# Performance work log

Hardware: AMD Instinct MI355X
Metric: run time of the kernel (lower is better)

## Reference

```python
import jax, jax.numpy as jnp
import numpy as np

D_MODEL, D_HID, N_EXPERTS, TOP_K = 1024, 4096, 8, 2

def setup_inputs() -> dict:
    key = jax.random.key(0)
    ks = jax.random.split(key, 6)
    B, T = 2, 2048
    x = jax.random.normal(ks[0], (B, T, D_MODEL), dtype=jnp.float32)
    gate_w = jax.random.normal(ks[1], (N_EXPERTS, D_MODEL), dtype=jnp.float32) * (1.0 / np.sqrt(D_MODEL))
    # kaiming_uniform-ish init for expert weights
    lim1 = np.sqrt(6.0 / D_MODEL)
    lim2 = np.sqrt(6.0 / D_HID)
    w1 = jax.random.uniform(ks[2], (N_EXPERTS, D_MODEL, D_HID), dtype=jnp.float32, minval=-lim1, maxval=lim1)
    w2 = jax.random.uniform(ks[3], (N_EXPERTS, D_HID, D_MODEL), dtype=jnp.float32, minval=-lim2, maxval=lim2)
    b1 = jnp.zeros((N_EXPERTS, 1, D_HID), dtype=jnp.float32)
    b2 = jnp.zeros((N_EXPERTS, 1, D_MODEL), dtype=jnp.float32)
    return {"x": x, "gate_w": gate_w, "w1": w1, "b1": b1, "w2": w2, "b2": b2}

def reference(x, gate_w, w1, b1, w2, b2):
    B, T, D = x.shape
    E = gate_w.shape[0]
    xf = x.reshape(-1, D)                              # [N, D]
    N = xf.shape[0]
    # Router: logits -> softmax -> top-k -> renormalize
    logits = jnp.einsum('nd,ed->ne', xf, gate_w)       # [N, E]
    scores = jax.nn.softmax(logits, axis=-1)
    top_w, top_i = jax.lax.top_k(scores, TOP_K)        # [N, K]
    top_w = top_w / jnp.sum(top_w, axis=-1, keepdims=True)
    # Dense combine weights (zero for unselected experts) — same math as
    # the padded-bmm dispatch/combine: padded slots have weight 0.
    gates = jnp.zeros((N, E), xf.dtype).at[jnp.arange(N)[:, None], top_i].add(top_w)  # [N, E]
    # Grouped expert MLP (computed densely; weighted combine zeroes unrouted experts)
    h = jax.nn.gelu(jnp.einsum('nd,edh->enh', xf, w1) + b1, approximate=False)  # [E, N, H]
    expert_out = jnp.einsum('enh,ehd->end', h, w2) + b2                          # [E, N, D]
    out = jnp.einsum('end,ne->nd', expert_out, gates)                            # [N, D]
    return out.reshape(B, T, D)
```

## Files before the change

kernel.cpp:

```cpp
#include <hip/hip_runtime.h>
#include <math.h>

#define NTOK 4096
#define DM   1024
#define DH   4096
#define NE   8
#define NSLOT (NTOK*2)
#define TMAX 72

typedef unsigned short u16;
typedef __attribute__((ext_vector_type(8))) short shortx8;
typedef __attribute__((ext_vector_type(4))) float floatx4;
typedef __attribute__((ext_vector_type(4))) int   intx4;

__device__ __forceinline__ u16 f2bf(float f) {
  union { float f; unsigned u; } c; c.f = f;
  unsigned r = c.u + 0x7fffu + ((c.u >> 16) & 1u);
  return (u16)(r >> 16);
}

__device__ __forceinline__ void async_cp16(const u16* g, u16* l) {
  __builtin_amdgcn_global_load_lds(
      (const __attribute__((address_space(1))) void*)g,
      (__attribute__((address_space(3))) void*)l, 16, 0, 0);
}

__global__ void cvt_x_kernel(const float* __restrict__ x, u16* __restrict__ xb) {
  int i = (blockIdx.x * 256 + threadIdx.x) * 8;
  float4 v0 = *(const float4*)(x + i);
  float4 v1 = *(const float4*)(x + i + 4);
  u16 tmp[8] = {f2bf(v0.x), f2bf(v0.y), f2bf(v0.z), f2bf(v0.w),
                f2bf(v1.x), f2bf(v1.y), f2bf(v1.z), f2bf(v1.w)};
  *(intx4*)(xb + i) = *(intx4*)tmp;
}

template<int K, int NW>
__global__ __launch_bounds__(256) void transpose_kernel(const float* __restrict__ W,
                                                        u16* __restrict__ Wt) {
  __shared__ u16 tile[64][66];
  int e = blockIdx.z;
  int n0 = blockIdx.x * 64, k0 = blockIdx.y * 64;
  int tt = threadIdx.x;
  const float* src = W + (size_t)e * K * NW + (size_t)(k0 + (tt >> 2)) * NW + n0 + (tt & 3) * 16;
  int r = tt >> 2, c4 = (tt & 3) * 16;
  float4 v[4];
#pragma unroll
  for (int i = 0; i < 4; i++) v[i] = *(const float4*)(src + i * 4);
#pragma unroll
  for (int i = 0; i < 4; i++) {
    tile[r][c4 + 4 * i + 0] = f2bf(v[i].x);
    tile[r][c4 + 4 * i + 1] = f2bf(v[i].y);
    tile[r][c4 + 4 * i + 2] = f2bf(v[i].z);
    tile[r][c4 + 4 * i + 3] = f2bf(v[i].w);
  }
  __syncthreads();
  u16* dst = Wt + (size_t)e * NW * K + (size_t)n0 * K + k0;
#pragma unroll
  for (int p = 0; p < 2; p++) {
    int n = (tt >> 3) + p * 32;
    int kc = (tt & 7) * 8;
    u16 o[8];
#pragma unroll
    for (int i = 0; i < 8; i++) o[i] = tile[kc + i][n];
    *(intx4*)(dst + (size_t)n * K + kc) = *(intx4*)o;
  }
}

__global__ __launch_bounds__(256) void router_kernel(const float* __restrict__ x,
                                                     const float* __restrict__ gw,
                                                     int* __restrict__ eos,
                                                     float* __restrict__ wos) {
  int wave = threadIdx.x >> 6, lane = threadIdx.x & 63;
  int n = blockIdx.x * 4 + wave;
  const float* xr = x + (size_t)n * DM;
  float acc[NE];
#pragma unroll
  for (int e = 0; e < NE; e++) acc[e] = 0.f;
  for (int d = lane; d < DM; d += 64) {
    float xv = xr[d];
#pragma unroll
    for (int e = 0; e < NE; e++) acc[e] += xv * gw[e * DM + d];
  }
#pragma unroll
  for (int e = 0; e < NE; e++) {
    float v = acc[e];
#pragma unroll
    for (int off = 32; off > 0; off >>= 1) v += __shfl_xor(v, off, 64);
    acc[e] = v;
  }
  if (lane == 0) {
    int i0 = 0;
    for (int e = 1; e < NE; e++) if (acc[e] > acc[i0]) i0 = e;
    int i1 = (i0 == 0) ? 1 : 0;
    for (int e = 0; e < NE; e++) { if (e == i0) continue; if (acc[e] > acc[i1]) i1 = e; }
    float e1 = expf(acc[i1] - acc[i0]);
    float w0 = 1.f / (1.f + e1);
    eos[2 * n] = i0;  eos[2 * n + 1] = i1;
    wos[2 * n] = w0;  wos[2 * n + 1] = 1.f - w0;
  }
}

__global__ __launch_bounds__(256) void build_groups_kernel(
    const int* __restrict__ eos, const float* __restrict__ wos,
    int* __restrict__ goff, int* __restrict__ tok_of_g, float* __restrict__ w_of_g,
    int* __restrict__ tiles, int* __restrict__ ntiles) {
  __shared__ int pref[256][NE];
  __shared__ int tot[NE];
  __shared__ int ebase[NE + 1];
  int t = threadIdx.x;
  int c[NE];
#pragma unroll
  for (int e = 0; e < NE; e++) c[e] = 0;
  for (int i = 0; i < NSLOT / 256; i++) {
    int e = eos[t * (NSLOT / 256) + i];
#pragma unroll
    for (int q = 0; q < NE; q++) if (e == q) c[q]++;
  }
#pragma unroll
  for (int e = 0; e < NE; e++) pref[t][e] = c[e];
  __syncthreads();
  if (t < NE) {
    int run = 0;
    for (int i = 0; i < 256; i++) { int v = pref[i][t]; pref[i][t] = run; run += v; }
    tot[t] = run;
  }
  __syncthreads();
  if (t == 0) {
    int o = 0;
    for (int e = 0; e < NE; e++) { ebase[e] = o; o += tot[e]; }
    ebase[NE] = o;
    int nt = 0;
    for (int e = 0; e < NE; e++)
      for (int mb = 0; mb * 128 < tot[e]; mb++) tiles[nt++] = (e << 16) | mb;
    ntiles[0] = nt;
  }
  __syncthreads();
  int off[NE];
#pragma unroll
  for (int e = 0; e < NE; e++) off[e] = ebase[e] + pref[t][e];
  for (int i = 0; i < NSLOT / 256; i++) {
    int s = t * (NSLOT / 256) + i;
    int e = eos[s];
    int g = 0;
#pragma unroll
    for (int q = 0; q < NE; q++) if (e == q) { g = off[q]; off[q] = g + 1; }
    tok_of_g[g] = s >> 1;
    w_of_g[g] = wos[s];
  }
  if (t <= NE) goff[t] = ebase[t];
}

template<int K, int NOUT, int MODE, int KSPLIT>
__global__ __launch_bounds__(256) void moe_gemm(
    const u16* __restrict__ A, const u16* __restrict__ Wt, const float* __restrict__ bias,
    const int* __restrict__ goff, const int* __restrict__ tok_of_g,
    const float* __restrict__ w_of_g, const int* __restrict__ tiles,
    const int* __restrict__ ntiles,
    u16* __restrict__ Hout, float* __restrict__ Out) {
  const int KLEN = K / KSPLIT;
  const int NB = NOUT / 128;
  const int NWG = TMAX * NB * KSPLIT;
  int flat = blockIdx.x;
  int wgid = (flat & 7) * (NWG >> 3) + (flat >> 3);
  int nb   = wgid % NB;
  int rest = wgid / NB;
  int tl   = rest % TMAX;
  int kseg = rest / TMAX;
  if (tl >= ntiles[0]) return;
  int packed = tiles[tl];
  int e = packed >> 16;
  int mb = packed & 0xffff;
  int gb = goff[e];
  int cntE = goff[e + 1] - gb;
  int m0 = mb * 128;
  int mvalid = cntE - m0; if (mvalid > 128) mvalid = 128;
  int gbase = gb + m0;
  int n0 = nb * 128;
  int kbeg = kseg * KLEN;
  int tid = threadIdx.x;
  int lane = tid & 63, wave = tid >> 6;

  __shared__ __align__(16) u16 As[2][128 * 64];
  __shared__ __align__(16) u16 Bs[2][128 * 64];

  int gcol = (((lane & 7) ^ (lane >> 3)) * 8);
  const u16 *pA[4], *pB[4];
  const u16* wte = Wt + (size_t)e * NOUT * K;
#pragma unroll
  for (int i = 0; i < 4; i++) {
    int rw = wave * 32 + i * 8 + (lane >> 3);
    int cw = (rw < mvalid) ? rw : (mvalid - 1);
    if (MODE == 0) pA[i] = A + (size_t)tok_of_g[gbase + cw] * K + gcol;
    else           pA[i] = A + (size_t)(gbase + cw) * K + gcol;
    pB[i] = wte + (size_t)(n0 + rw) * K + gcol;
  }

  int wm = wave >> 1, wn = wave & 1;
  int lr = lane & 15;
  int c0 = (((lane >> 4)) ^ (lr & 7)) * 8;
  int c1 = ((4 + (lane >> 4)) ^ (lr & 7)) * 8;

  floatx4 acc[4][4];
#pragma unroll
  for (int i = 0; i < 4; i++)
#pragma unroll
    for (int j = 0; j < 4; j++) acc[i][j] = (floatx4){0.f, 0.f, 0.f, 0.f};

  auto stage = [&](int b, int k0) {
#pragma unroll
    for (int i = 0; i < 4; i++)
      async_cp16(pA[i] + k0, &As[b][(wave * 32 + i * 8) * 64]);
#pragma unroll
    for (int i = 0; i < 4; i++)
      async_cp16(pB[i] + k0, &Bs[b][(wave * 32 + i * 8) * 64]);
  };

  const int NT = KLEN / 64;
  stage(0, kbeg);
  stage(1, kbeg + 64);

  shortx8 af[8], bfr[8];
  auto ldfrag_half = [&](int b, int h) {
    int cc = h ? c1 : c0;
#pragma unroll
    for (int i = 0; i < 4; i++) {
      af[h * 4 + i]  = *(const shortx8*)&As[b][(wm * 64 + i * 16 + lr) * 64 + cc];
      bfr[h * 4 + i] = *(const shortx8*)&Bs[b][(wn * 64 + i * 16 + lr) * 64 + cc];
    }
  };
  auto mfma_half = [&](int h) {
#pragma unroll
    for (int i = 0; i < 4; i++)
#pragma unroll
      for (int j = 0; j < 4; j++)
        acc[i][j] = __builtin_amdgcn_mfma_f32_16x16x32_bf16(af[h * 4 + i], bfr[h * 4 + j],
                                                            acc[i][j], 0, 0, 0);
  };

  for (int t = 0; t < NT - 2; ++t) {
    int cur = t & 1;
    asm volatile("s_waitcnt vmcnt(8)" ::: "memory");
    __builtin_amdgcn_s_barrier();
    asm volatile("" ::: "memory");
    ldfrag_half(cur, 0);
    asm volatile("" ::: "memory");
    ldfrag_half(cur, 1);
    asm volatile("s_waitcnt lgkmcnt(8)" ::: "memory");
    __builtin_amdgcn_sched_barrier(0);
    __builtin_amdgcn_s_setprio(1);
    mfma_half(0);
    __builtin_amdgcn_s_setprio(0);
    asm volatile("s_waitcnt lgkmcnt(0)" ::: "memory");
    __builtin_amdgcn_sched_barrier(0);
    __builtin_amdgcn_s_barrier();
    __builtin_amdgcn_sched_barrier(0);
    stage(cur, kbeg + (t + 2) * 64);
    __builtin_amdgcn_sched_barrier(0);
    __builtin_amdgcn_s_setprio(1);
    mfma_half(1);
    __builtin_amdgcn_s_setprio(0);
  }
#pragma unroll
  for (int tt2 = 0; tt2 < 2; ++tt2) {
    int cur = (NT + tt2) & 1;
    if (tt2 == 0) asm volatile("s_waitcnt vmcnt(8)" ::: "memory");
    else          asm volatile("s_waitcnt vmcnt(0)" ::: "memory");
    __builtin_amdgcn_s_barrier();
    asm volatile("" ::: "memory");
    ldfrag_half(cur, 0);
    asm volatile("" ::: "memory");
    ldfrag_half(cur, 1);
    asm volatile("s_waitcnt lgkmcnt(8)" ::: "memory");
    __builtin_amdgcn_sched_barrier(0);
    mfma_half(0);
    asm volatile("s_waitcnt lgkmcnt(0)" ::: "memory");
    __builtin_amdgcn_sched_barrier(0);
    mfma_half(1);
  }

  const float* bp = bias + (size_t)e * NOUT + n0;
  if (MODE == 0) {
#pragma unroll
    for (int i = 0; i < 4; i++) {
      int rowb = wm * 64 + i * 16 + (lane >> 4) * 4;
#pragma unroll
      for (int r = 0; r < 4; r++) {
        int grow = rowb + r;
        if (grow < mvalid) {
          size_t base = (size_t)(gbase + grow) * NOUT + n0;
#pragma unroll
          for (int j = 0; j < 4; j++) {
            int col = wn * 64 + j * 16 + lr;
            float v = acc[i][j][r] + bp[col];
            v = 0.5f * v * (1.f + erff(v * 0.70710678118654752f));
            Hout[base + col] = f2bf(v);
          }
        }
      }
    }
  } else {
#pragma unroll
    for (int i = 0; i < 4; i++) {
      int rowb = wm * 64 + i * 16 + (lane >> 4) * 4;
#pragma unroll
      for (int r = 0; r < 4; r++) {
        int grow = rowb + r;
        if (grow < mvalid) {
          int gi = gbase + grow;
          int t = tok_of_g[gi];
          float wg = w_of_g[gi];
          float* orow = Out + (size_t)t * DM + n0;
#pragma unroll
          for (int j = 0; j < 4; j++) {
            int col = wn * 64 + j * 16 + lr;
            float bb = (kseg == 0) ? bp[col] : 0.f;
            atomicAdd(&orow[col], wg * (acc[i][j][r] + bb));
          }
        }
      }
    }
  }
}

extern "C" void kernel_launch(void* const* d_in, const int* in_sizes, int n_in,
                              void* d_out, int out_size, void* d_ws, size_t ws_size,
                              hipStream_t stream) {
  const float* x  = (const float*)d_in[0];
  const float* gw = (const float*)d_in[1];
  const float* w1 = (const float*)d_in[2];
  const float* b1 = (const float*)d_in[3];
  const float* w2 = (const float*)d_in[4];
  const float* b2 = (const float*)d_in[5];
  float* out = (float*)d_out;
  char* ws = (char*)d_ws;

  u16* xb = (u16*)(ws + 0);
  u16* wt = (u16*)(ws + 8388608);
  u16* h  = (u16*)(ws + 75497472);
  char* meta = ws + 142606336;
  int*   eos      = (int*)(meta);
  int*   tok_of_g = (int*)(meta + 32768);
  float* wos      = (float*)(meta + 65536);
  float* w_of_g   = (float*)(meta + 98304);
  int*   goff     = (int*)(meta + 131072);
  int*   tiles    = (int*)(meta + 131200);
  int*   ntiles   = (int*)(meta + 131584);

  hipMemsetAsync(out, 0, (size_t)NTOK * DM * 4, stream);

  cvt_x_kernel<<<NTOK * DM / 8 / 256, 256, 0, stream>>>(x, xb);
  transpose_kernel<DM, DH><<<dim3(DH / 64, DM / 64, NE), 256, 0, stream>>>(w1, wt);
  router_kernel<<<NTOK / 4, 256, 0, stream>>>(x, gw, eos, wos);
  build_groups_kernel<<<1, 256, 0, stream>>>(eos, wos, goff, tok_of_g, w_of_g, tiles, ntiles);
  moe_gemm<DM, DH, 0, 1><<<TMAX * (DH / 128), 256, 0, stream>>>(
      xb, wt, b1, goff, tok_of_g, w_of_g, tiles, ntiles, h, nullptr);
  transpose_kernel<DH, DM><<<dim3(DM / 64, DH / 64, NE), 256, 0, stream>>>(w2, wt);
  moe_gemm<DH, DM, 1, 2><<<TMAX * (DM / 128) * 2, 256, 0, stream>>>(
      h, wt, b2, goff, tok_of_g, w_of_g, tiles, ntiles, nullptr, out);
}
```

Baseline: 714.7 us.

## Enlarge MoE GEMM tiles to 256x256 with 512-thread workgroups

```diff
diff --git a/kernel.cpp b/kernel.cpp
--- a/kernel.cpp
+++ b/kernel.cpp
@@ -6,7 +6,7 @@
 #define DH   4096
 #define NE   8
 #define NSLOT (NTOK*2)
-#define TMAX 72
+#define TM   40
 
 typedef unsigned short u16;
 typedef __attribute__((ext_vector_type(8))) short shortx8;
@@ -131,7 +131,7 @@
     ebase[NE] = o;
     int nt = 0;
     for (int e = 0; e < NE; e++)
-      for (int mb = 0; mb * 128 < tot[e]; mb++) tiles[nt++] = (e << 16) | mb;
+      for (int mb = 0; mb * 256 < tot[e]; mb++) tiles[nt++] = (e << 16) | mb;
     ntiles[0] = nt;
   }
   __syncthreads();
@@ -151,37 +151,37 @@
 }
 
 template<int K, int NOUT, int MODE, int KSPLIT>
-__global__ __launch_bounds__(256) void moe_gemm(
+__global__ __launch_bounds__(512, 2) void moe_gemm(
     const u16* __restrict__ A, const u16* __restrict__ Wt, const float* __restrict__ bias,
     const int* __restrict__ goff, const int* __restrict__ tok_of_g,
     const float* __restrict__ w_of_g, const int* __restrict__ tiles,
     const int* __restrict__ ntiles,
     u16* __restrict__ Hout, float* __restrict__ Out) {
   const int KLEN = K / KSPLIT;
-  const int NB = NOUT / 128;
-  const int NWG = TMAX * NB * KSPLIT;
+  const int NB = NOUT / 256;
+  const int NWG = TM * NB * KSPLIT;
   int flat = blockIdx.x;
   int wgid = (flat & 7) * (NWG >> 3) + (flat >> 3);
   int nb   = wgid % NB;
   int rest = wgid / NB;
-  int tl   = rest % TMAX;
-  int kseg = rest / TMAX;
+  int tl   = rest % TM;
+  int kseg = rest / TM;
   if (tl >= ntiles[0]) return;
   int packed = tiles[tl];
   int e = packed >> 16;
   int mb = packed & 0xffff;
   int gb = goff[e];
   int cntE = goff[e + 1] - gb;
-  int m0 = mb * 128;
-  int mvalid = cntE - m0; if (mvalid > 128) mvalid = 128;
+  int m0 = mb * 256;
+  int mvalid = cntE - m0; if (mvalid > 256) mvalid = 256;
   int gbase = gb + m0;
-  int n0 = nb * 128;
+  int n0 = nb * 256;
   int kbeg = kseg * KLEN;
   int tid = threadIdx.x;
   int lane = tid & 63, wave = tid >> 6;
 
-  __shared__ __align__(16) u16 As[2][128 * 64];
-  __shared__ __align__(16) u16 Bs[2][128 * 64];
+  __shared__ __align__(16) u16 As[2][256 * 64];
+  __shared__ __align__(16) u16 Bs[2][256 * 64];
 
   int gcol = (((lane & 7) ^ (lane >> 3)) * 8);
   const u16 *pA[4], *pB[4];
@@ -195,14 +195,14 @@
     pB[i] = wte + (size_t)(n0 + rw) * K + gcol;
   }
 
-  int wm = wave >> 1, wn = wave & 1;
+  int wm = wave >> 2, wn = wave & 3;
   int lr = lane & 15;
   int c0 = (((lane >> 4)) ^ (lr & 7)) * 8;
   int c1 = ((4 + (lane >> 4)) ^ (lr & 7)) * 8;
 
-  floatx4 acc[4][4];
-#pragma unroll
-  for (int i = 0; i < 4; i++)
+  floatx4 acc[8][4];
+#pragma unroll
+  for (int i = 0; i < 8; i++)
 #pragma unroll
     for (int j = 0; j < 4; j++) acc[i][j] = (floatx4){0.f, 0.f, 0.f, 0.f};
 
@@ -219,22 +219,22 @@
   stage(0, kbeg);
   stage(1, kbeg + 64);
 
-  shortx8 af[8], bfr[8];
+  shortx8 af[8], bfr[4];
   auto ldfrag_half = [&](int b, int h) {
     int cc = h ? c1 : c0;
 #pragma unroll
-    for (int i = 0; i < 4; i++) {
-      af[h * 4 + i]  = *(const shortx8*)&As[b][(wm * 64 + i * 16 + lr) * 64 + cc];
-      bfr[h * 4 + i] = *(const shortx8*)&Bs[b][(wn * 64 + i * 16 + lr) * 64 + cc];
-    }
+    for (int i = 0; i < 8; i++)
+      af[i]  = *(const shortx8*)&As[b][(wm * 128 + i * 16 + lr) * 64 + cc];
+#pragma unroll
+    for (int j = 0; j < 4; j++)
+      bfr[j] = *(const shortx8*)&Bs[b][(wn * 64 + j * 16 + lr) * 64 + cc];
   };
-  auto mfma_half = [&](int h) {
-#pragma unroll
-    for (int i = 0; i < 4; i++)
+  auto mfma_half = [&]() {
+#pragma unroll
+    for (int i = 0; i < 8; i++)
 #pragma unroll
       for (int j = 0; j < 4; j++)
-        acc[i][j] = __builtin_amdgcn_mfma_f32_16x16x32_bf16(af[h * 4 + i], bfr[h * 4 + j],
-                                                            acc[i][j], 0, 0, 0);
+        acc[i][j] = __builtin_amdgcn_mfma_f32_16x16x32_bf16(af[i], bfr[j], acc[i][j], 0, 0, 0);
   };
 
   for (int t = 0; t < NT - 2; ++t) {
@@ -243,21 +243,20 @@
     __builtin_amdgcn_s_barrier();
     asm volatile("" ::: "memory");
     ldfrag_half(cur, 0);
-    asm volatile("" ::: "memory");
+    asm volatile("s_waitcnt lgkmcnt(0)" ::: "memory");
+    __builtin_amdgcn_sched_barrier(0);
+    __builtin_amdgcn_s_setprio(1);
+    mfma_half();
+    __builtin_amdgcn_s_setprio(0);
     ldfrag_half(cur, 1);
-    asm volatile("s_waitcnt lgkmcnt(8)" ::: "memory");
+    asm volatile("s_waitcnt lgkmcnt(0)" ::: "memory");
+    __builtin_amdgcn_sched_barrier(0);
+    __builtin_amdgcn_s_barrier();
+    __builtin_amdgcn_sched_barrier(0);
+    stage(cur, kbeg + (t + 2) * 64);
     __builtin_amdgcn_sched_barrier(0);
     __builtin_amdgcn_s_setprio(1);
-    mfma_half(0);
-    __builtin_amdgcn_s_setprio(0);
-    asm volatile("s_waitcnt lgkmcnt(0)" ::: "memory");
-    __builtin_amdgcn_sched_barrier(0);
-    __builtin_amdgcn_s_barrier();
-    __builtin_amdgcn_sched_barrier(0);
-    stage(cur, kbeg + (t + 2) * 64);
-    __builtin_amdgcn_sched_barrier(0);
-    __builtin_amdgcn_s_setprio(1);
-    mfma_half(1);
+    mfma_half();
     __builtin_amdgcn_s_setprio(0);
   }
 #pragma unroll
@@ -268,21 +267,20 @@
     __builtin_amdgcn_s_barrier();
     asm volatile("" ::: "memory");
     ldfrag_half(cur, 0);
-    asm volatile("" ::: "memory");
+    asm volatile("s_waitcnt lgkmcnt(0)" ::: "memory");
+    __builtin_amdgcn_sched_barrier(0);
+    mfma_half();
     ldfrag_half(cur, 1);
-    asm volatile("s_waitcnt lgkmcnt(8)" ::: "memory");
-    __builtin_amdgcn_sched_barrier(0);
-    mfma_half(0);
     asm volatile("s_waitcnt lgkmcnt(0)" ::: "memory");
     __builtin_amdgcn_sched_barrier(0);
-    mfma_half(1);
+    mfma_half();
   }
 
   const float* bp = bias + (size_t)e * NOUT + n0;
   if (MODE == 0) {
 #pragma unroll
-    for (int i = 0; i < 4; i++) {
-      int rowb = wm * 64 + i * 16 + (lane >> 4) * 4;
+    for (int i = 0; i < 8; i++) {
+      int rowb = wm * 128 + i * 16 + (lane >> 4) * 4;
 #pragma unroll
       for (int r = 0; r < 4; r++) {
         int grow = rowb + r;
@@ -300,8 +298,8 @@
     }
   } else {
 #pragma unroll
-    for (int i = 0; i < 4; i++) {
-      int rowb = wm * 64 + i * 16 + (lane >> 4) * 4;
+    for (int i = 0; i < 8; i++) {
+      int rowb = wm * 128 + i * 16 + (lane >> 4) * 4;
 #pragma unroll
       for (int r = 0; r < 4; r++) {
         int grow = rowb + r;
@@ -352,9 +350,9 @@
   transpose_kernel<DM, DH><<<dim3(DH / 64, DM / 64, NE), 256, 0, stream>>>(w1, wt);
   router_kernel<<<NTOK / 4, 256, 0, stream>>>(x, gw, eos, wos);
   build_groups_kernel<<<1, 256, 0, stream>>>(eos, wos, goff, tok_of_g, w_of_g, tiles, ntiles);
-  moe_gemm<DM, DH, 0, 1><<<TMAX * (DH / 128), 256, 0, stream>>>(
+  moe_gemm<DM, DH, 0, 1><<<TM * (DH / 256), 512, 0, stream>>>(
       xb, wt, b1, goff, tok_of_g, w_of_g, tiles, ntiles, h, nullptr);
   transpose_kernel<DH, DM><<<dim3(DM / 64, DH / 64, NE), 256, 0, stream>>>(w2, wt);
-  moe_gemm<DH, DM, 1, 2><<<TMAX * (DM / 128) * 2, 256, 0, stream>>>(
+  moe_gemm<DH, DM, 1, 4><<<TM * (DM / 256) * 4, 512, 0, stream>>>(
       h, wt, b2, goff, tok_of_g, w_of_g, tiles, ntiles, nullptr, out);
 }
```

New measurement: 780.6 us. +9.2%, slower.
